# Kernel optimization log

Measured on AMD Instinct MI355X. Metric: run time of the kernel, lower is better.

The kernel has to match this reference:

```python
import jax, jax.numpy as jnp
import numpy as np

NUM_EXPERTS = 64


def setup_inputs() -> dict:
    key = jax.random.key(0)
    k1, k2 = jax.random.split(key)
    x = jax.random.normal(k1, (8192, 4096), dtype=jnp.float32)
    W = jax.random.normal(k2, (NUM_EXPERTS, 4096), dtype=jnp.float32) * 0.02
    return {"x": x, "W": W}


def reference(x, W):
    # gate: logits = x @ W^T  -> [T, E]
    logits = jnp.einsum('th,eh->te', x, W)
    scores = jax.nn.softmax(logits, axis=-1)
    # top_k == 1 path: max with keepdim (torch scores.max(dim=-1, keepdim=True))
    expert_weights = jnp.max(scores, axis=-1, keepdims=True)      # [T, 1]
    expert_indices = jnp.argmax(scores, axis=-1, keepdims=True)   # [T, 1] int
    # routing_counts = bincount(expert_indices.squeeze(1), minlength=E)
    routing_counts = jnp.bincount(expert_indices[:, 0], length=NUM_EXPERTS)
    return (expert_weights, expert_indices, scores, routing_counts)
```

## Files before the change

### kernel.cpp

```cpp
#include <hip/hip_runtime.h>
#include <stdint.h>

#define T_TOKENS 8192
#define K_DIM    4096
#define NEXP     64
#define TB       128
#define KC       32

typedef short bf16x8 __attribute__((ext_vector_type(8)));
typedef float f32x4  __attribute__((ext_vector_type(4)));

__device__ __forceinline__ uint32_t f2bf(float v) {
    uint32_t u = __builtin_bit_cast(uint32_t, v);
    return (u + 0x7fffu + ((u >> 16) & 1u)) >> 16;
}
__device__ __forceinline__ float bf2f(uint32_t b) {
    return __builtin_bit_cast(float, b << 16);
}

__global__ void wpack(const float* __restrict__ W, float4* __restrict__ Wf,
                      float* __restrict__ out_counts) {
    const int l     = threadIdx.x;
    const int kstep = blockIdx.x;
    const int etile = blockIdx.y;
    if (kstep == 0 && etile == 0)
        out_counts[l] = 0.f;
    const int e = etile * 16 + (l & 15);
    const int k = kstep * 32 + (l >> 4) * 8;
    const float* src = W + (size_t)e * K_DIM + k;
    bf16x8 h, l1, l2;
#pragma unroll
    for (int j = 0; j < 8; ++j) {
        float v = src[j];
        uint32_t hb = f2bf(v); float r  = v - bf2f(hb);
        uint32_t lb = f2bf(r); float r2 = r - bf2f(lb);
        uint32_t qb = f2bf(r2);
        h[j] = (short)hb; l1[j] = (short)lb; l2[j] = (short)qb;
    }
    const size_t base = ((size_t)(kstep * 4 + etile) * 3) * 64 + l;
    Wf[base]       = __builtin_bit_cast(float4, h);
    Wf[base + 64]  = __builtin_bit_cast(float4, l1);
    Wf[base + 128] = __builtin_bit_cast(float4, l2);
}

__global__ __launch_bounds__(512, 4) void gemm_mfma(
    const float*  __restrict__ x,
    const float4* __restrict__ Wf,
    float* __restrict__ P,
    int KS)
{
    __shared__ float4 xbuf[2][TB * 8];
    __shared__ float4 bbuf[2][12 * 64];

    const int tid  = threadIdx.x;
    const int l    = tid & 63;
    const int wv   = __builtin_amdgcn_readfirstlane(tid >> 6);
    const int t0   = blockIdx.x * TB;
    const int slice = blockIdx.y;
    const int k0   = slice * KS;
    const int nchunk = KS / KC;

    const int srow  = tid >> 3;
    const int sslot = tid & 7;
    const float4* x4 = (const float4*)x;
    const size_t xg0 = (size_t)(t0 + srow) * (K_DIM / 4) + (size_t)(k0 >> 2) + sslot;
    const size_t xg1 = xg0 + (size_t)64 * (K_DIM / 4);
    const size_t bg0 = ((size_t)(k0 / 32)) * 768;

    f32x4 acc[4];
#pragma unroll
    for (int et = 0; et < 4; ++et) acc[et] = (f32x4){0.f, 0.f, 0.f, 0.f};

    float4 xr0 = x4[xg0];
    float4 xr1 = x4[xg1];
    float4 br0 = Wf[bg0 + tid];
    float4 br1 = (tid < 256) ? Wf[bg0 + tid + 512] : (float4){0, 0, 0, 0};

    const int arow = wv * 16 + (l & 15);
    const int as0 = arow * 8 + (((l >> 4) * 2)     ^ (arow & 7));
    const int as1 = arow * 8 + (((l >> 4) * 2 + 1) ^ (arow & 7));

    for (int c = 0; c < nchunk; ++c) {
        const int b = c & 1;
        xbuf[b][srow * 8        + (sslot ^ (srow & 7))]        = xr0;
        xbuf[b][(srow + 64) * 8 + (sslot ^ ((srow + 64) & 7))] = xr1;
        bbuf[b][tid] = br0;
        if (tid < 256) bbuf[b][tid + 512] = br1;
        __syncthreads();

        if (c + 1 < nchunk) {
            xr0 = x4[xg0 + (size_t)(c + 1) * 8];
            xr1 = x4[xg1 + (size_t)(c + 1) * 8];
            br0 = Wf[bg0 + (size_t)(c + 1) * 768 + tid];
            if (tid < 256) br1 = Wf[bg0 + (size_t)(c + 1) * 768 + tid + 512];
        }

        float4 a0 = xbuf[b][as0];
        float4 a1 = xbuf[b][as1];
        float av[8] = {a0.x, a0.y, a0.z, a0.w, a1.x, a1.y, a1.z, a1.w};
        bf16x8 xh, xl, xq;
#pragma unroll
        for (int j = 0; j < 8; ++j) {
            float v = av[j];
            uint32_t hb = f2bf(v); float r  = v - bf2f(hb);
            uint32_t lb = f2bf(r); float r2 = r - bf2f(lb);
            uint32_t qb = f2bf(r2);
            xh[j] = (short)hb; xl[j] = (short)lb; xq[j] = (short)qb;
        }

#pragma unroll
        for (int et = 0; et < 4; ++et) {
            const float4* bp = &bbuf[b][et * 3 * 64 + l];
            bf16x8 wh = __builtin_bit_cast(bf16x8, bp[0]);
            bf16x8 wl = __builtin_bit_cast(bf16x8, bp[64]);
            bf16x8 wq = __builtin_bit_cast(bf16x8, bp[128]);
            acc[et] = __builtin_amdgcn_mfma_f32_16x16x32_bf16(xh, wh, acc[et], 0, 0, 0);
            acc[et] = __builtin_amdgcn_mfma_f32_16x16x32_bf16(xh, wl, acc[et], 0, 0, 0);
            acc[et] = __builtin_amdgcn_mfma_f32_16x16x32_bf16(xh, wq, acc[et], 0, 0, 0);
            acc[et] = __builtin_amdgcn_mfma_f32_16x16x32_bf16(xl, wh, acc[et], 0, 0, 0);
            acc[et] = __builtin_amdgcn_mfma_f32_16x16x32_bf16(xl, wl, acc[et], 0, 0, 0);
            acc[et] = __builtin_amdgcn_mfma_f32_16x16x32_bf16(xq, wh, acc[et], 0, 0, 0);
        }
    }

    float* Pp = P + (size_t)slice * T_TOKENS * NEXP;
#pragma unroll
    for (int et = 0; et < 4; ++et) {
#pragma unroll
        for (int i = 0; i < 4; ++i) {
            int t = t0 + wv * 16 + (l >> 4) * 4 + i;
            Pp[(size_t)t * NEXP + et * 16 + (l & 15)] = acc[et][i];
        }
    }
}

__global__ __launch_bounds__(256) void router_finish(
    const float* __restrict__ P, float* __restrict__ out, int S)
{
    const int lane = threadIdx.x & 63;
    const int wv   = threadIdx.x >> 6;
    const int t    = blockIdx.x * 4 + wv;

    float lg = 0.f;
    for (int s = 0; s < S; ++s)
        lg += P[((size_t)s * T_TOKENS + t) * NEXP + lane];

    float* out_w = out;
    float* out_i = out + T_TOKENS;
    float* out_s = out + 2 * T_TOKENS;
    float* out_c = out + 2 * T_TOKENS + (size_t)T_TOKENS * NEXP;

    float m = lg;
#pragma unroll
    for (int off = 32; off > 0; off >>= 1)
        m = fmaxf(m, __shfl_xor(m, off));
    float p = expf(lg - m);
    float s = p;
#pragma unroll
    for (int off = 32; off > 0; off >>= 1)
        s += __shfl_xor(s, off);
    float sc = p / s;

    float bv = sc; int bi = lane;
#pragma unroll
    for (int off = 32; off > 0; off >>= 1) {
        float ov = __shfl_xor(bv, off);
        int   oi = __shfl_xor(bi, off);
        if (ov > bv || (ov == bv && oi < bi)) { bv = ov; bi = oi; }
    }
    out_s[(size_t)t * NEXP + lane] = sc;
    if (lane == 0) {
        out_w[t] = bv;
        out_i[t] = (float)bi;
        atomicAdd(&out_c[bi], 1.0f);
    }
}

extern "C" void kernel_launch(void* const* d_in, const int* in_sizes, int n_in,
                              void* d_out, int out_size, void* d_ws, size_t ws_size,
                              hipStream_t stream)
{
    const float* x = (const float*)d_in[0];
    const float* W = (const float*)d_in[1];
    float* out = (float*)d_out;
    float* out_s = out + 2 * T_TOKENS;
    float* out_c = out + 2 * T_TOKENS + (size_t)T_TOKENS * NEXP;

    const size_t wf_bytes  = (size_t)128 * 4 * 3 * 64 * 16;
    const size_t per_slice = (size_t)T_TOKENS * NEXP * sizeof(float);

    int S = 8;
    while (S > 1 && wf_bytes + (size_t)S * per_slice > ws_size) S >>= 1;
    float4* Wf = (float4*)d_ws;
    float* Pbuf;
    if (wf_bytes + per_slice <= ws_size) {
        Pbuf = (float*)((char*)d_ws + wf_bytes);
    } else {
        S = 1;
        Pbuf = out_s;
    }

    wpack<<<dim3(128, 4), 64, 0, stream>>>(W, Wf, out_c);
    gemm_mfma<<<dim3(T_TOKENS / TB, S), 512, 0, stream>>>(x, Wf, Pbuf, K_DIM / S);
    router_finish<<<T_TOKENS / 4, 256, 0, stream>>>(Pbuf, out, S);
}
```

Before: 94.76 us.

## Load x directly into MFMA registers, double K chunk, template finish kernel

The GEMM kernel no longer stages x through shared memory. Each lane loads its MFMA A-operand fragments straight from global memory into registers and prefetches the next chunk. The K chunk doubles to 64, so there are half as many barriers and the weight tile in LDS doubles. The router finish kernel is templated on the split count so its reduction loop unrolls. The trade-off is uncoalesced-ish 32-byte-per-lane global loads for x, plus more registers that may reduce occupancy.

```diff
diff --git a/kernel.cpp b/kernel.cpp
--- a/kernel.cpp
+++ b/kernel.cpp
@@ -5,7 +5,7 @@
 #define K_DIM    4096
 #define NEXP     64
 #define TB       128
-#define KC       32
+#define KC       64
 
 typedef short bf16x8 __attribute__((ext_vector_type(8)));
 typedef float f32x4  __attribute__((ext_vector_type(4)));
@@ -16,6 +16,19 @@
 }
 __device__ __forceinline__ float bf2f(uint32_t b) {
     return __builtin_bit_cast(float, b << 16);
+}
+
+__device__ __forceinline__ void cvt3(const float4 a0, const float4 a1,
+                                     bf16x8& xh, bf16x8& xl, bf16x8& xq) {
+    const float av[8] = {a0.x, a0.y, a0.z, a0.w, a1.x, a1.y, a1.z, a1.w};
+#pragma unroll
+    for (int j = 0; j < 8; ++j) {
+        float v = av[j];
+        uint32_t hb = f2bf(v); float r  = v - bf2f(hb);
+        uint32_t lb = f2bf(r); float r2 = r - bf2f(lb);
+        uint32_t qb = f2bf(r2);
+        xh[j] = (short)hb; xl[j] = (short)lb; xq[j] = (short)qb;
+    }
 }
 
 __global__ void wpack(const float* __restrict__ W, float4* __restrict__ Wf,
@@ -49,8 +62,7 @@
     float* __restrict__ P,
     int KS)
 {
-    __shared__ float4 xbuf[2][TB * 8];
-    __shared__ float4 bbuf[2][12 * 64];
+    __shared__ float4 bbuf[2][1536];
 
     const int tid  = threadIdx.x;
     const int l    = tid & 63;
@@ -60,67 +72,72 @@
     const int k0   = slice * KS;
     const int nchunk = KS / KC;
 
-    const int srow  = tid >> 3;
-    const int sslot = tid & 7;
     const float4* x4 = (const float4*)x;
-    const size_t xg0 = (size_t)(t0 + srow) * (K_DIM / 4) + (size_t)(k0 >> 2) + sslot;
-    const size_t xg1 = xg0 + (size_t)64 * (K_DIM / 4);
-    const size_t bg0 = ((size_t)(k0 / 32)) * 768;
+    const int arow = wv * 16 + (l & 15);
+    const size_t xg = (size_t)(t0 + arow) * (K_DIM / 4) + (size_t)(k0 >> 2) + ((l >> 4) * 2);
+
+    const size_t bg0 = ((size_t)(k0 >> 5)) * 768;
 
     f32x4 acc[4];
 #pragma unroll
     for (int et = 0; et < 4; ++et) acc[et] = (f32x4){0.f, 0.f, 0.f, 0.f};
 
-    float4 xr0 = x4[xg0];
-    float4 xr1 = x4[xg1];
     float4 br0 = Wf[bg0 + tid];
-    float4 br1 = (tid < 256) ? Wf[bg0 + tid + 512] : (float4){0, 0, 0, 0};
-
-    const int arow = wv * 16 + (l & 15);
-    const int as0 = arow * 8 + (((l >> 4) * 2)     ^ (arow & 7));
-    const int as1 = arow * 8 + (((l >> 4) * 2 + 1) ^ (arow & 7));
+    float4 br1 = Wf[bg0 + tid + 512];
+    float4 br2 = Wf[bg0 + tid + 1024];
+    float4 xa0 = x4[xg + 0], xa1 = x4[xg + 1];
+    float4 xa2 = x4[xg + 8], xa3 = x4[xg + 9];
 
     for (int c = 0; c < nchunk; ++c) {
         const int b = c & 1;
-        xbuf[b][srow * 8        + (sslot ^ (srow & 7))]        = xr0;
-        xbuf[b][(srow + 64) * 8 + (sslot ^ ((srow + 64) & 7))] = xr1;
-        bbuf[b][tid] = br0;
-        if (tid < 256) bbuf[b][tid + 512] = br1;
+        bbuf[b][tid]        = br0;
+        bbuf[b][tid + 512]  = br1;
+        bbuf[b][tid + 1024] = br2;
         __syncthreads();
 
+        float4 xn0 = xa0, xn1 = xa1, xn2 = xa2, xn3 = xa3;
         if (c + 1 < nchunk) {
-            xr0 = x4[xg0 + (size_t)(c + 1) * 8];
-            xr1 = x4[xg1 + (size_t)(c + 1) * 8];
-            br0 = Wf[bg0 + (size_t)(c + 1) * 768 + tid];
-            if (tid < 256) br1 = Wf[bg0 + (size_t)(c + 1) * 768 + tid + 512];
+            const size_t bo = bg0 + (size_t)(c + 1) * 1536;
+            br0 = Wf[bo + tid];
+            br1 = Wf[bo + tid + 512];
+            br2 = Wf[bo + tid + 1024];
+            const size_t xo = xg + (size_t)(c + 1) * 16;
+            xn0 = x4[xo + 0]; xn1 = x4[xo + 1];
+            xn2 = x4[xo + 8]; xn3 = x4[xo + 9];
         }
 
-        float4 a0 = xbuf[b][as0];
-        float4 a1 = xbuf[b][as1];
-        float av[8] = {a0.x, a0.y, a0.z, a0.w, a1.x, a1.y, a1.z, a1.w};
-        bf16x8 xh, xl, xq;
-#pragma unroll
-        for (int j = 0; j < 8; ++j) {
-            float v = av[j];
-            uint32_t hb = f2bf(v); float r  = v - bf2f(hb);
-            uint32_t lb = f2bf(r); float r2 = r - bf2f(lb);
-            uint32_t qb = f2bf(r2);
-            xh[j] = (short)hb; xl[j] = (short)lb; xq[j] = (short)qb;
+        bf16x8 xh0, xl0, xq0, xh1, xl1, xq1;
+        cvt3(xa0, xa1, xh0, xl0, xq0);
+        cvt3(xa2, xa3, xh1, xl1, xq1);
+
+#pragma unroll
+        for (int et = 0; et < 4; ++et) {
+            {
+                const float4* bp = &bbuf[b][et * 192 + l];
+                bf16x8 wh = __builtin_bit_cast(bf16x8, bp[0]);
+                bf16x8 wl = __builtin_bit_cast(bf16x8, bp[64]);
+                bf16x8 wq = __builtin_bit_cast(bf16x8, bp[128]);
+                acc[et] = __builtin_amdgcn_mfma_f32_16x16x32_bf16(xh0, wh, acc[et], 0, 0, 0);
+                acc[et] = __builtin_amdgcn_mfma_f32_16x16x32_bf16(xh0, wl, acc[et], 0, 0, 0);
+                acc[et] = __builtin_amdgcn_mfma_f32_16x16x32_bf16(xh0, wq, acc[et], 0, 0, 0);
+                acc[et] = __builtin_amdgcn_mfma_f32_16x16x32_bf16(xl0, wh, acc[et], 0, 0, 0);
+                acc[et] = __builtin_amdgcn_mfma_f32_16x16x32_bf16(xl0, wl, acc[et], 0, 0, 0);
+                acc[et] = __builtin_amdgcn_mfma_f32_16x16x32_bf16(xq0, wh, acc[et], 0, 0, 0);
+            }
+            {
+                const float4* bp = &bbuf[b][768 + et * 192 + l];
+                bf16x8 wh = __builtin_bit_cast(bf16x8, bp[0]);
+                bf16x8 wl = __builtin_bit_cast(bf16x8, bp[64]);
+                bf16x8 wq = __builtin_bit_cast(bf16x8, bp[128]);
+                acc[et] = __builtin_amdgcn_mfma_f32_16x16x32_bf16(xh1, wh, acc[et], 0, 0, 0);
+                acc[et] = __builtin_amdgcn_mfma_f32_16x16x32_bf16(xh1, wl, acc[et], 0, 0, 0);
+                acc[et] = __builtin_amdgcn_mfma_f32_16x16x32_bf16(xh1, wq, acc[et], 0, 0, 0);
+                acc[et] = __builtin_amdgcn_mfma_f32_16x16x32_bf16(xl1, wh, acc[et], 0, 0, 0);
+                acc[et] = __builtin_amdgcn_mfma_f32_16x16x32_bf16(xl1, wl, acc[et], 0, 0, 0);
+                acc[et] = __builtin_amdgcn_mfma_f32_16x16x32_bf16(xq1, wh, acc[et], 0, 0, 0);
+            }
         }
-
-#pragma unroll
-        for (int et = 0; et < 4; ++et) {
-            const float4* bp = &bbuf[b][et * 3 * 64 + l];
-            bf16x8 wh = __builtin_bit_cast(bf16x8, bp[0]);
-            bf16x8 wl = __builtin_bit_cast(bf16x8, bp[64]);
-            bf16x8 wq = __builtin_bit_cast(bf16x8, bp[128]);
-            acc[et] = __builtin_amdgcn_mfma_f32_16x16x32_bf16(xh, wh, acc[et], 0, 0, 0);
-            acc[et] = __builtin_amdgcn_mfma_f32_16x16x32_bf16(xh, wl, acc[et], 0, 0, 0);
-            acc[et] = __builtin_amdgcn_mfma_f32_16x16x32_bf16(xh, wq, acc[et], 0, 0, 0);
-            acc[et] = __builtin_amdgcn_mfma_f32_16x16x32_bf16(xl, wh, acc[et], 0, 0, 0);
-            acc[et] = __builtin_amdgcn_mfma_f32_16x16x32_bf16(xl, wl, acc[et], 0, 0, 0);
-            acc[et] = __builtin_amdgcn_mfma_f32_16x16x32_bf16(xq, wh, acc[et], 0, 0, 0);
-        }
+        xa0 = xn0; xa1 = xn1; xa2 = xn2; xa3 = xn3;
     }
 
     float* Pp = P + (size_t)slice * T_TOKENS * NEXP;
@@ -134,14 +151,16 @@
     }
 }
 
-__global__ __launch_bounds__(256) void router_finish(
-    const float* __restrict__ P, float* __restrict__ out, int S)
+template <int S>
+__global__ __launch_bounds__(256) void router_finish_t(
+    const float* __restrict__ P, float* __restrict__ out)
 {
     const int lane = threadIdx.x & 63;
     const int wv   = threadIdx.x >> 6;
     const int t    = blockIdx.x * 4 + wv;
 
     float lg = 0.f;
+#pragma unroll
     for (int s = 0; s < S; ++s)
         lg += P[((size_t)s * T_TOKENS + t) * NEXP + lane];
 
@@ -202,5 +221,10 @@
 
     wpack<<<dim3(128, 4), 64, 0, stream>>>(W, Wf, out_c);
     gemm_mfma<<<dim3(T_TOKENS / TB, S), 512, 0, stream>>>(x, Wf, Pbuf, K_DIM / S);
-    router_finish<<<T_TOKENS / 4, 256, 0, stream>>>(Pbuf, out, S);
-}
+    switch (S) {
+        case 8: router_finish_t<8><<<T_TOKENS / 4, 256, 0, stream>>>(Pbuf, out); break;
+        case 4: router_finish_t<4><<<T_TOKENS / 4, 256, 0, stream>>>(Pbuf, out); break;
+        case 2: router_finish_t<2><<<T_TOKENS / 4, 256, 0, stream>>>(Pbuf, out); break;
+        default: router_finish_t<1><<<T_TOKENS / 4, 256, 0, stream>>>(Pbuf, out); break;
+    }
+}
```

After: 94.61 us. Within noise of the previous version (-0.2%).
